# Optimization experiments

Hardware: AMD Instinct MI355X
Metric: run time of the kernel (lower is better)

The kernel has to match this reference:

```python
import jax, jax.numpy as jnp
import numpy as np

BITS = 4
MASK = (1 << BITS) - 1  # 15
GROUP_SIZE = 128
IN_F, OUT_F = 4096, 11008
N_GROUPS = IN_F // GROUP_SIZE  # 32
PACK = 32 // BITS  # 8 nibbles per int32


def setup_inputs() -> dict:
    key = jax.random.key(0)
    k1, k2, k3, k4, k5 = jax.random.split(key, 5)
    x = jax.random.normal(k1, (64, IN_F), dtype=jnp.float32)
    # arbitrary packed int4 payloads: random 32-bit patterns viewed as int32
    qweight = jax.lax.bitcast_convert_type(
        jax.random.bits(k2, (IN_F // 32 * BITS, OUT_F), dtype=jnp.uint32), jnp.int32)
    qzeros = jax.lax.bitcast_convert_type(
        jax.random.bits(k3, (N_GROUPS, OUT_F // 32 * BITS), dtype=jnp.uint32), jnp.int32)
    scales = (jax.random.uniform(k4, (N_GROUPS, OUT_F), dtype=jnp.float32) + 0.1) * 0.01
    g_idx = (jnp.arange(IN_F, dtype=jnp.int32) // GROUP_SIZE).astype(jnp.int32)
    bias = jax.random.normal(k5, (OUT_F,), dtype=jnp.float32)
    return {"x": x, "qweight": qweight, "qzeros": qzeros,
            "scales": scales, "g_idx": g_idx, "bias": bias}


def reference(x, qweight, qzeros, scales, g_idx, bias):
    wf = jnp.arange(0, 32, BITS, dtype=jnp.int32)  # [8] shift amounts
    # unpack zero points: [n_groups, out/8, 8] -> [n_groups, out]
    zeros = (jnp.right_shift(qzeros[:, :, None], wf[None, None, :]) & MASK) + 1
    zeros = zeros.reshape(scales.shape).astype(scales.dtype)
    # unpack weights: [in/8, 8, out] -> [in, out]
    w = jnp.right_shift(qweight[:, None, :], wf[None, :, None]) & MASK
    w = w.reshape(-1, qweight.shape[1]).astype(scales.dtype)
    # per-group dequant, then dense matmul
    W = scales[g_idx] * (w - zeros[g_idx])  # [in, out]
    out = jnp.matmul(x, W).astype(x.dtype) + bias.astype(x.dtype)
    return out
```

## Files before the change

kernel.cpp:

```cpp
#include <hip/hip_runtime.h>

#define IN_F 4096
#define OUT_F 11008
#define M_ROWS 64
#define KSPLIT 8
#define GPB 4
#define NT_BLK 128
#define NBLK_N (OUT_F / NT_BLK)
#define QZ_WORDS (OUT_F / 8)

typedef __attribute__((ext_vector_type(8))) short short8;
typedef __attribute__((ext_vector_type(4))) float float4v;

__device__ __forceinline__ short f2bf(float f) {
    unsigned u = __builtin_bit_cast(unsigned, f);
    return (short)((u + 0x7FFFu + ((u >> 16) & 1u)) >> 16);
}
__device__ __forceinline__ short f2bf_t(float f) {
    return (short)(__builtin_bit_cast(unsigned, f) >> 16);
}

__global__ __launch_bounds__(256) void cvt_kernel(const float* __restrict__ x,
                                                  short* __restrict__ xbf2) {
    const int T = blockIdx.x * 256 + threadIdx.x;
    const int u = T >> 6, m = T & 63;
    const float* src = x + m * IN_F + u * 8;
    float4v f0 = *(const float4v*)src;
    float4v f1 = *(const float4v*)(src + 4);
    short8 h;
#pragma unroll
    for (int j = 0; j < 4; ++j) {
        h[j]     = f2bf(f0[j]);
        h[j + 4] = f2bf(f1[j]);
    }
    *(short8*)(xbf2 + T * 8) = h;
}

__global__ __launch_bounds__(256, 2) void qlin_kernel(
    const short* __restrict__ xbf2,
    const int*   __restrict__ qweight,
    const int*   __restrict__ qzeros,
    const float* __restrict__ scales,
    const float* __restrict__ bias,
    float* __restrict__ out)
{
    __shared__ short lds_a[2][16][64][8];

    const int blk  = blockIdx.x;
    const int nb   = blk % NBLK_N;
    const int kg   = blk / NBLK_N;
    const int t    = threadIdx.x;
    const int wave = t >> 6;
    const int lane = t & 63;
    const int q    = lane >> 4;
    const int nl   = lane & 15;
    const int n0   = nb * NT_BLK + wave * 32 + nl;
    const int n1   = n0 + 16;
    const int shz  = (n0 & 7) * 4;
    const int g0   = kg * GPB;

    float4v acc0[4], acc1[4];
#pragma unroll
    for (int i = 0; i < 4; ++i) {
        acc0[i] = (float4v){0.f, 0.f, 0.f, 0.f};
        acc1[i] = (float4v){0.f, 0.f, 0.f, 0.f};
    }

#define STAGE(buf, g)                                                          \
    {                                                                          \
        _Pragma("unroll")                                                      \
        for (int i_ = 0; i_ < 4; ++i_) {                                       \
            const int u_ = wave * 4 + i_;                                      \
            const short* gsrc_ = xbf2 + (((g) * 16 + u_) * 64 + lane) * 8;     \
            __builtin_amdgcn_global_load_lds(                                  \
                (const __attribute__((address_space(1))) void*)gsrc_,          \
                (__attribute__((address_space(3))) void*)&lds_a[buf][u_][0][0],\
                16, 0, 0);                                                     \
        }                                                                      \
    }

#define LOAD_META(g, qw, zw0, zw1, s0v, s1v)                                   \
    {                                                                          \
        _Pragma("unroll")                                                      \
        for (int kk_ = 0; kk_ < 4; ++kk_) {                                    \
            const int row_ = (g) * 16 + kk_ * 4 + q;                           \
            qw[kk_]     = qweight[row_ * OUT_F + n0];                          \
            qw[kk_ + 4] = qweight[row_ * OUT_F + n1];                          \
        }                                                                      \
        zw0 = qzeros[(g) * QZ_WORDS + (n0 >> 3)];                              \
        zw1 = qzeros[(g) * QZ_WORDS + (n1 >> 3)];                              \
        s0v = scales[(g) * OUT_F + n0];                                        \
        s1v = scales[(g) * OUT_F + n1];                                        \
    }

    int qwc[8], zc0, zc1;
    float sc0, sc1;
    STAGE(0, g0);
    LOAD_META(g0, qwc, zc0, zc1, sc0, sc1);

#pragma unroll
    for (int gi = 0; gi < GPB; ++gi) {
        __syncthreads();

        int qwn[8], zn0, zn1;
        float sn0, sn1;
        if (gi + 1 < GPB) {
            STAGE((gi + 1) & 1, g0 + gi + 1);
            LOAD_META(g0 + gi + 1, qwn, zn0, zn1, sn0, sn1);
        }

        const float s0  = sc0, s1 = sc1;
        const float nz0 = -s0 * (float)(((zc0 >> shz) & 15) + 1);
        const float nz1 = -s1 * (float)(((zc1 >> shz) & 15) + 1);

#pragma unroll
        for (int kk = 0; kk < 4; ++kk) {
            short8 b0, b1;
#pragma unroll
            for (int j = 0; j < 8; ++j) {
                b0[j] = f2bf_t(fmaf(s0, (float)((qwc[kk] >> (4 * j)) & 15), nz0));
                b1[j] = f2bf_t(fmaf(s1, (float)((qwc[kk + 4] >> (4 * j)) & 15), nz1));
            }
            const int u = kk * 4 + q;
#pragma unroll
            for (int mt = 0; mt < 4; ++mt) {
                short8 a = *(const short8*)&lds_a[gi & 1][u][mt * 16 + nl][0];
                acc0[mt] = __builtin_amdgcn_mfma_f32_16x16x32_bf16(a, b0, acc0[mt], 0, 0, 0);
                acc1[mt] = __builtin_amdgcn_mfma_f32_16x16x32_bf16(a, b1, acc1[mt], 0, 0, 0);
            }
        }

        if (gi + 1 < GPB) {
#pragma unroll
            for (int i = 0; i < 8; ++i) qwc[i] = qwn[i];
            zc0 = zn0; zc1 = zn1; sc0 = sn0; sc1 = sn1;
        }
    }

    const float bv0 = (kg == 0) ? bias[n0] : 0.f;
    const float bv1 = (kg == 0) ? bias[n1] : 0.f;
#pragma unroll
    for (int mt = 0; mt < 4; ++mt) {
#pragma unroll
        for (int r = 0; r < 4; ++r) {
            const int m = mt * 16 + q * 4 + r;
            atomicAdd(&out[m * OUT_F + n0], acc0[mt][r] + bv0);
            atomicAdd(&out[m * OUT_F + n1], acc1[mt][r] + bv1);
        }
    }
#undef STAGE
#undef LOAD_META
}

extern "C" void kernel_launch(void* const* d_in, const int* in_sizes, int n_in,
                              void* d_out, int out_size, void* d_ws, size_t ws_size,
                              hipStream_t stream) {
    const float* x       = (const float*)d_in[0];
    const int*   qweight = (const int*)d_in[1];
    const int*   qzeros  = (const int*)d_in[2];
    const float* scales  = (const float*)d_in[3];
    const float* bias    = (const float*)d_in[5];
    float* out = (float*)d_out;
    short* xbf2 = (short*)d_ws;

    hipMemsetAsync(out, 0, (size_t)M_ROWS * OUT_F * sizeof(float), stream);
    cvt_kernel<<<dim3((IN_F / 8) * M_ROWS / 256), dim3(256), 0, stream>>>(x, xbf2);
    qlin_kernel<<<dim3(NBLK_N * KSPLIT), dim3(256), 0, stream>>>(
        xbf2, qweight, qzeros, scales, bias, out);
}
```

Before: 102.4 us.

## Replace atomic split-K reduction with bf16 partial buffers and separate reduce kernel

Each split-K block now writes its partial sums as bf16 into a per-split workspace slice instead of doing float atomicAdds into a zeroed output. A new reduce kernel sums the eight slices, adds the bias and writes the output, which also removes the memset. The main kernel also stops staging activations through LDS with double buffering and reads them straight from global memory, and raises the occupancy hint to 3 blocks. Rounding the partials to bf16 costs accuracy, and the direct global loads give up the prefetch overlap of weights and metadata that the old loop had.

```diff
diff --git a/kernel.cpp b/kernel.cpp
--- a/kernel.cpp
+++ b/kernel.cpp
@@ -8,6 +8,7 @@
 #define NT_BLK 128
 #define NBLK_N (OUT_F / NT_BLK)
 #define QZ_WORDS (OUT_F / 8)
+#define SLICE (M_ROWS * OUT_F)
 
 typedef __attribute__((ext_vector_type(8))) short short8;
 typedef __attribute__((ext_vector_type(4))) float float4v;
@@ -18,6 +19,9 @@
 }
 __device__ __forceinline__ short f2bf_t(float f) {
     return (short)(__builtin_bit_cast(unsigned, f) >> 16);
+}
+__device__ __forceinline__ float bf2f(short h) {
+    return __builtin_bit_cast(float, ((unsigned)(unsigned short)h) << 16);
 }
 
 __global__ __launch_bounds__(256) void cvt_kernel(const float* __restrict__ x,
@@ -36,16 +40,13 @@
     *(short8*)(xbf2 + T * 8) = h;
 }
 
-__global__ __launch_bounds__(256, 2) void qlin_kernel(
+__global__ __launch_bounds__(256, 3) void qlin_kernel(
     const short* __restrict__ xbf2,
     const int*   __restrict__ qweight,
     const int*   __restrict__ qzeros,
     const float* __restrict__ scales,
-    const float* __restrict__ bias,
-    float* __restrict__ out)
+    short* __restrict__ part)
 {
-    __shared__ short lds_a[2][16][64][8];
-
     const int blk  = blockIdx.x;
     const int nb   = blk % NBLK_N;
     const int kg   = blk / NBLK_N;
@@ -66,90 +67,71 @@
         acc1[i] = (float4v){0.f, 0.f, 0.f, 0.f};
     }
 
-#define STAGE(buf, g)                                                          \
-    {                                                                          \
-        _Pragma("unroll")                                                      \
-        for (int i_ = 0; i_ < 4; ++i_) {                                       \
-            const int u_ = wave * 4 + i_;                                      \
-            const short* gsrc_ = xbf2 + (((g) * 16 + u_) * 64 + lane) * 8;     \
-            __builtin_amdgcn_global_load_lds(                                  \
-                (const __attribute__((address_space(1))) void*)gsrc_,          \
-                (__attribute__((address_space(3))) void*)&lds_a[buf][u_][0][0],\
-                16, 0, 0);                                                     \
-        }                                                                      \
-    }
-
-#define LOAD_META(g, qw, zw0, zw1, s0v, s1v)                                   \
-    {                                                                          \
-        _Pragma("unroll")                                                      \
-        for (int kk_ = 0; kk_ < 4; ++kk_) {                                    \
-            const int row_ = (g) * 16 + kk_ * 4 + q;                           \
-            qw[kk_]     = qweight[row_ * OUT_F + n0];                          \
-            qw[kk_ + 4] = qweight[row_ * OUT_F + n1];                          \
-        }                                                                      \
-        zw0 = qzeros[(g) * QZ_WORDS + (n0 >> 3)];                              \
-        zw1 = qzeros[(g) * QZ_WORDS + (n1 >> 3)];                              \
-        s0v = scales[(g) * OUT_F + n0];                                        \
-        s1v = scales[(g) * OUT_F + n1];                                        \
-    }
-
-    int qwc[8], zc0, zc1;
-    float sc0, sc1;
-    STAGE(0, g0);
-    LOAD_META(g0, qwc, zc0, zc1, sc0, sc1);
+    const short* abase_nl = xbf2 + nl * 8;
 
 #pragma unroll
     for (int gi = 0; gi < GPB; ++gi) {
-        __syncthreads();
+        const int g = g0 + gi;
 
-        int qwn[8], zn0, zn1;
-        float sn0, sn1;
-        if (gi + 1 < GPB) {
-            STAGE((gi + 1) & 1, g0 + gi + 1);
-            LOAD_META(g0 + gi + 1, qwn, zn0, zn1, sn0, sn1);
+        int qw[8];
+#pragma unroll
+        for (int kk = 0; kk < 4; ++kk) {
+            const int row = g * 16 + kk * 4 + q;
+            qw[kk]     = qweight[row * OUT_F + n0];
+            qw[kk + 4] = qweight[row * OUT_F + n1];
         }
-
-        const float s0  = sc0, s1 = sc1;
-        const float nz0 = -s0 * (float)(((zc0 >> shz) & 15) + 1);
-        const float nz1 = -s1 * (float)(((zc1 >> shz) & 15) + 1);
+        const float s0  = scales[g * OUT_F + n0];
+        const float s1  = scales[g * OUT_F + n1];
+        const float nz0 = -s0 * (float)(((qzeros[g * QZ_WORDS + (n0 >> 3)] >> shz) & 15) + 1);
+        const float nz1 = -s1 * (float)(((qzeros[g * QZ_WORDS + (n1 >> 3)] >> shz) & 15) + 1);
 
 #pragma unroll
         for (int kk = 0; kk < 4; ++kk) {
             short8 b0, b1;
 #pragma unroll
             for (int j = 0; j < 8; ++j) {
-                b0[j] = f2bf_t(fmaf(s0, (float)((qwc[kk] >> (4 * j)) & 15), nz0));
-                b1[j] = f2bf_t(fmaf(s1, (float)((qwc[kk + 4] >> (4 * j)) & 15), nz1));
+                b0[j] = f2bf_t(fmaf(s0, (float)((qw[kk] >> (4 * j)) & 15), nz0));
+                b1[j] = f2bf_t(fmaf(s1, (float)((qw[kk + 4] >> (4 * j)) & 15), nz1));
             }
             const int u = kk * 4 + q;
+            const short* abase = abase_nl + (g * 16 + u) * 64 * 8;
 #pragma unroll
             for (int mt = 0; mt < 4; ++mt) {
-                short8 a = *(const short8*)&lds_a[gi & 1][u][mt * 16 + nl][0];
+                short8 a = *(const short8*)(abase + mt * 16 * 8);
                 acc0[mt] = __builtin_amdgcn_mfma_f32_16x16x32_bf16(a, b0, acc0[mt], 0, 0, 0);
                 acc1[mt] = __builtin_amdgcn_mfma_f32_16x16x32_bf16(a, b1, acc1[mt], 0, 0, 0);
             }
         }
-
-        if (gi + 1 < GPB) {
-#pragma unroll
-            for (int i = 0; i < 8; ++i) qwc[i] = qwn[i];
-            zc0 = zn0; zc1 = zn1; sc0 = sn0; sc1 = sn1;
-        }
     }
 
-    const float bv0 = (kg == 0) ? bias[n0] : 0.f;
-    const float bv1 = (kg == 0) ? bias[n1] : 0.f;
+    short* myp = part + kg * SLICE;
 #pragma unroll
     for (int mt = 0; mt < 4; ++mt) {
 #pragma unroll
         for (int r = 0; r < 4; ++r) {
             const int m = mt * 16 + q * 4 + r;
-            atomicAdd(&out[m * OUT_F + n0], acc0[mt][r] + bv0);
-            atomicAdd(&out[m * OUT_F + n1], acc1[mt][r] + bv1);
+            myp[m * OUT_F + n0] = f2bf(acc0[mt][r]);
+            myp[m * OUT_F + n1] = f2bf(acc1[mt][r]);
         }
     }
-#undef STAGE
-#undef LOAD_META
+}
+
+__global__ __launch_bounds__(256) void reduce_kernel(
+    const short* __restrict__ part, const float* __restrict__ bias,
+    float* __restrict__ out) {
+    const int i8 = (blockIdx.x * 256 + threadIdx.x) * 8;
+    const int n  = i8 % OUT_F;
+    float s[8];
+#pragma unroll
+    for (int j = 0; j < 8; ++j) s[j] = bias[n + j];
+#pragma unroll
+    for (int kg = 0; kg < KSPLIT; ++kg) {
+        short8 p = *(const short8*)(part + kg * SLICE + i8);
+#pragma unroll
+        for (int j = 0; j < 8; ++j) s[j] += bf2f(p[j]);
+    }
+    *(float4v*)(out + i8)     = (float4v){s[0], s[1], s[2], s[3]};
+    *(float4v*)(out + i8 + 4) = (float4v){s[4], s[5], s[6], s[7]};
 }
 
 extern "C" void kernel_launch(void* const* d_in, const int* in_sizes, int n_in,
@@ -161,10 +143,12 @@
     const float* scales  = (const float*)d_in[3];
     const float* bias    = (const float*)d_in[5];
     float* out = (float*)d_out;
+
     short* xbf2 = (short*)d_ws;
+    short* part = (short*)((char*)d_ws + (1 << 20));
 
-    hipMemsetAsync(out, 0, (size_t)M_ROWS * OUT_F * sizeof(float), stream);
     cvt_kernel<<<dim3((IN_F / 8) * M_ROWS / 256), dim3(256), 0, stream>>>(x, xbf2);
     qlin_kernel<<<dim3(NBLK_N * KSPLIT), dim3(256), 0, stream>>>(
-        xbf2, qweight, qzeros, scales, bias, out);
+        xbf2, qweight, qzeros, scales, part);
+    reduce_kernel<<<dim3(SLICE / 8 / 256), dim3(256), 0, stream>>>(part, bias, out);
 }
```

Result: faster. 95.91 us (-6.4%).
